# Kernel tuning notes

Hardware: AMD Instinct MI355X
Metric: run time of the kernel (lower is better)

Reference implementation:

```python
import jax, jax.numpy as jnp
import numpy as np

B, S = 1, 1024
V_SZ, D, L, H, DK, DV = 50304, 768, 12, 24, 32, 32
EPS = 1e-5


def layernorm(x, g, b):
    m = jnp.mean(x, axis=-1, keepdims=True)
    v = jnp.mean((x - m) ** 2, axis=-1, keepdims=True)
    return (x - m) * jax.lax.rsqrt(v + EPS) * g + b


def setup_inputs() -> dict:
    key = jax.random.key(0)
    ks = jax.random.split(key, 8)
    s = 0.02
    qkv_out = H * (DK + DK + DV)
    return {
        "token_ids": jax.random.randint(ks[0], (B, S), 0, V_SZ),
        "embed_w": (jax.random.uniform(ks[1], (V_SZ, D), minval=-1.0, maxval=1.0) / np.float32(np.sqrt(D))).astype(jnp.float32),
        "pos_w": jax.random.normal(ks[2], (D, 2 * D), dtype=jnp.float32) * s,
        "pos_b": jnp.zeros((2 * D,), jnp.float32),
        "ln1_g": jnp.ones((L, D), jnp.float32),
        "ln1_b": jnp.zeros((L, D), jnp.float32),
        "qkv_w": jax.random.normal(ks[3], (L, D, qkv_out), dtype=jnp.float32) * s,
        "qkv_b": jnp.zeros((L, qkv_out), jnp.float32),
        "ff_w1": jax.random.normal(ks[4], (L, H * DV, 2 * D), dtype=jnp.float32) * s,
        "ff_b1": jnp.zeros((L, 2 * D), jnp.float32),
        "ff_w2": jax.random.normal(ks[5], (L, D, D), dtype=jnp.float32) * s,
        "lnf_g": jnp.ones((D,), jnp.float32),
        "lnf_b": jnp.zeros((D,), jnp.float32),
    }


def _embed_position(x, pos_w, pos_b):
    # Heinsen log-linear recurrence (arXiv:2311.06281), using_prev_context=False.
    h = x @ pos_w + pos_b                     # [B,S,2D]
    log_coeffs = jax.nn.log_sigmoid(h[..., :D])
    logits = h[..., D:]
    a_star = jnp.pad(jnp.cumsum(log_coeffs, axis=1), ((0, 0), (1, 0), (0, 0)))  # [B,S+1,D]
    prepended = jnp.pad(logits, ((0, 0), (1, 0), (0, 0)))                        # logit0 = 0
    rec = a_star + jax.lax.cumlogsumexp(prepended - a_star, axis=1)
    return x + rec[:, 1:, :]


def _layer(x, p):
    g1, b1, wqkv, bqkv, w1, bb1, w2 = p
    y = layernorm(x, g1, b1) @ wqkv + bqkv                  # [B,S,H*(2DK+DV)]
    y = y.reshape(B, S, H, DK + DK + DV).transpose(0, 2, 1, 3)  # [B,H,S,.]
    Q, K, V = y[..., :DK], y[..., DK:2 * DK], y[..., 2 * DK:]
    # Heinsen log-domain causal attention (arXiv:2404.05843)
    H_S = jax.lax.cumlogsumexp(K[..., :, None] + V[..., None, :], axis=2)  # [B,H,S,DK,DV]
    H_Z = jax.lax.cumlogsumexp(K, axis=2)                                   # [B,H,S,DK]
    log_S = jax.nn.logsumexp(Q[..., None] + H_S, axis=-2)                   # [B,H,S,DV]
    log_Z = jax.nn.logsumexp(Q + H_Z, axis=-1, keepdims=True)               # [B,H,S,1]
    att = (log_S - log_Z).transpose(0, 2, 1, 3).reshape(B, S, H * DV)
    z = att @ w1 + bb1                                       # [B,S,2D]
    z = z[..., :D] * jax.nn.sigmoid(z[..., D:])              # GLU(dim=-1)
    z = z @ w2
    return x + z, None


def reference(token_ids, embed_w, pos_w, pos_b, ln1_g, ln1_b, qkv_w, qkv_b, ff_w1, ff_b1, ff_w2, lnf_g, lnf_b):
    x = embed_w[token_ids]                                   # [B,S,D]
    x = _embed_position(x, pos_w, pos_b)
    x, _ = jax.lax.scan(_layer, x, (ln1_g, ln1_b, qkv_w, qkv_b, ff_w1, ff_b1, ff_w2))
    x = layernorm(x, lnf_g, lnf_b)
    return x @ embed_w.T                                     # [B,S,V_SZ]
```

## Files before the change

kernel.cpp:

```cpp
#include <hip/hip_runtime.h>
#include <math.h>

#define S 1024
#define D 768
#define L 12
#define NH 24
#define QKV_OUT 2304
#define FF1_OUT 1536
#define V_SZ 50304

typedef unsigned short u16;
typedef __attribute__((ext_vector_type(8))) short bf16x8;
typedef __attribute__((ext_vector_type(4))) float f32x4;

__device__ __forceinline__ u16 f2bf(float x) {
    unsigned u = __float_as_uint(x);
    u += 0x7fffu + ((u >> 16) & 1u);
    return (u16)(u >> 16);
}

__device__ __forceinline__ void async_copy16(const void* g, void* l) {
    __builtin_amdgcn_global_load_lds(
        (const __attribute__((address_space(1))) unsigned int*)g,
        (__attribute__((address_space(3))) unsigned int*)l, 16, 0, 0);
}

__global__ __launch_bounds__(256) void embed_kernel(
    const int* __restrict__ tok, const float* __restrict__ ew,
    float* __restrict__ x, u16* __restrict__ xb) {
    int t = blockIdx.x;
    int id = tok[t];
    const float* src = ew + (size_t)id * D;
    for (int d = threadIdx.x; d < D; d += 256) {
        float v = src[d];
        x[(size_t)t * D + d] = v;
        xb[(size_t)t * D + d] = f2bf(v);
    }
}

__global__ __launch_bounds__(256) void cvt_bf16_kernel(
    const float* __restrict__ in, u16* __restrict__ out) {
    size_t i = ((size_t)blockIdx.x * 256 + threadIdx.x) * 8;
    float4 a = *(const float4*)(in + i);
    float4 b = *(const float4*)(in + i + 4);
    uint4 o;
    o.x = (unsigned)f2bf(a.x) | ((unsigned)f2bf(a.y) << 16);
    o.y = (unsigned)f2bf(a.z) | ((unsigned)f2bf(a.w) << 16);
    o.z = (unsigned)f2bf(b.x) | ((unsigned)f2bf(b.y) << 16);
    o.w = (unsigned)f2bf(b.z) | ((unsigned)f2bf(b.w) << 16);
    *(uint4*)(out + i) = o;
}

__global__ __launch_bounds__(256) void pos_scan_kernel(
    const float* __restrict__ h, float* __restrict__ x) {
    const int d = blockIdx.x;
    const int tid = threadIdx.x;
    float a[4], b[4];
    #pragma unroll
    for (int i = 0; i < 4; ++i) {
        int t = tid * 4 + i;
        float g  = h[(size_t)t * FF1_OUT + d];
        float lg = h[(size_t)t * FF1_OUT + D + d];
        a[i] = 1.f / (1.f + __expf(-g));
        b[i] = __expf(lg);
    }
    float A = ((a[0] * a[1]) * a[2]) * a[3];
    float B = ((b[0] * a[1] + b[1]) * a[2] + b[2]) * a[3] + b[3];

    __shared__ float sA[256], sB[256];
    sA[tid] = A; sB[tid] = B;
    __syncthreads();
    #pragma unroll
    for (int off = 1; off < 256; off <<= 1) {
        float selfA = sA[tid], selfB = sB[tid];
        float pA = 1.f, pB = 0.f;
        if (tid >= off) { pA = sA[tid - off]; pB = sB[tid - off]; }
        __syncthreads();
        sA[tid] = pA * selfA;
        sB[tid] = pB * selfA + selfB;
        __syncthreads();
    }
    float R = 1.f;
    if (tid > 0) R = sA[tid - 1] + sB[tid - 1];
    #pragma unroll
    for (int i = 0; i < 4; ++i) {
        R = R * a[i] + b[i];
        x[(size_t)(tid * 4 + i) * D + d] += __logf(R);
    }
}

__global__ __launch_bounds__(256) void ln_kernel(
    const float* __restrict__ in, const float* __restrict__ g,
    const float* __restrict__ b, u16* __restrict__ out) {
    int row = blockIdx.x;
    int tid = threadIdx.x;
    const float* p = in + (size_t)row * D;
    float v0 = p[tid], v1 = p[tid + 256], v2 = p[tid + 512];

    __shared__ float red[8];
    float s = v0 + v1 + v2;
    #pragma unroll
    for (int o = 32; o > 0; o >>= 1) s += __shfl_down(s, o, 64);
    int wave = tid >> 6, lane = tid & 63;
    if (lane == 0) red[wave] = s;
    __syncthreads();
    float mean = (red[0] + red[1] + red[2] + red[3]) * (1.f / (float)D);

    float d0 = v0 - mean, d1 = v1 - mean, d2 = v2 - mean;
    float ss = d0 * d0 + d1 * d1 + d2 * d2;
    #pragma unroll
    for (int o = 32; o > 0; o >>= 1) ss += __shfl_down(ss, o, 64);
    if (lane == 0) red[4 + wave] = ss;
    __syncthreads();
    float var = (red[4] + red[5] + red[6] + red[7]) * (1.f / (float)D);
    float rstd = rsqrtf(var + 1e-5f);

    u16* o = out + (size_t)row * D;
    o[tid]       = f2bf(d0 * rstd * g[tid]       + b[tid]);
    o[tid + 256] = f2bf(d1 * rstd * g[tid + 256] + b[tid + 256]);
    o[tid + 512] = f2bf(d2 * rstd * g[tid + 512] + b[tid + 512]);
}

__global__ __launch_bounds__(256) void wconv_kernel(
    const float* __restrict__ W, u16* __restrict__ WT, int N) {
    __shared__ float tile[32][33];
    const int z = blockIdx.z;
    W  += (size_t)z * 768 * N;
    WT += (size_t)z * N * 768;
    const int n0 = blockIdx.x * 32, k0 = blockIdx.y * 32;
    const int t = threadIdx.x;
    const int r = t >> 3, c4 = (t & 7) * 4;
    float4 v = *(const float4*)(W + (size_t)(k0 + r) * N + n0 + c4);
    tile[r][c4] = v.x; tile[r][c4 + 1] = v.y; tile[r][c4 + 2] = v.z; tile[r][c4 + 3] = v.w;
    __syncthreads();
    ushort4 o;
    o.x = f2bf(tile[c4][r]);     o.y = f2bf(tile[c4 + 1][r]);
    o.z = f2bf(tile[c4 + 2][r]); o.w = f2bf(tile[c4 + 3][r]);
    *(ushort4*)(WT + (size_t)(n0 + r) * 768 + k0 + c4) = o;
}

template <bool XSWZ>
__global__ __launch_bounds__(256) void gemm_bf16_kernel(
    const u16* __restrict__ A, const u16* __restrict__ B,
    const float* __restrict__ bias, const float* __restrict__ Cin,
    float* __restrict__ C, int N) {
    constexpr int K = 768;
    __shared__ __align__(16) u16 As[128 * 32];
    __shared__ __align__(16) u16 Bs[128 * 32];
    const int tid = threadIdx.x;
    const int w = tid >> 6, lane = tid & 63;
    int m0, n0;
    if (XSWZ) {
        const int lid = blockIdx.x;
        const int xcd = lid & 7, local = lid >> 3;
        const int work = xcd * 393 + local;
        n0 = (work >> 3) * 128;
        m0 = (work & 7) * 128;
    } else {
        m0 = blockIdx.y * 128;
        n0 = blockIdx.x * 128;
    }
    const int wm = (w >> 1) * 64, wn = (w & 1) * 64;

    f32x4 acc[4][4] = {};

    const int rA = w * 32 + (lane >> 2);
    const int cA = (lane & 3) * 8;
    const int frow = lane & 15;
    const int fko = (lane >> 4) * 8;

    for (int k0 = 0; k0 < K; k0 += 32) {
        {
            const u16* g0 = A + (size_t)(m0 + rA) * K + k0 + cA;
            async_copy16(g0, (char*)As + w * 2048);
            async_copy16(g0 + (size_t)16 * K, (char*)As + w * 2048 + 1024);
        }
        {
            const u16* g0 = B + (size_t)(n0 + rA) * K + k0 + cA;
            async_copy16(g0, (char*)Bs + w * 2048);
            async_copy16(g0 + (size_t)16 * K, (char*)Bs + w * 2048 + 1024);
        }
        __syncthreads();

        bf16x8 af[4], bfr[4];
        #pragma unroll
        for (int i = 0; i < 4; ++i)
            af[i] = *(const bf16x8*)(As + (wm + i * 16 + frow) * 32 + fko);
        #pragma unroll
        for (int j = 0; j < 4; ++j)
            bfr[j] = *(const bf16x8*)(Bs + (wn + j * 16 + frow) * 32 + fko);
        #pragma unroll
        for (int i = 0; i < 4; ++i)
            #pragma unroll
            for (int j = 0; j < 4; ++j)
                acc[i][j] = __builtin_amdgcn_mfma_f32_16x16x32_bf16(af[i], bfr[j], acc[i][j], 0, 0, 0);
        __syncthreads();
    }

    const int crow = wm + (lane >> 4) * 4;
    const int ccol = wn + (lane & 15);
    #pragma unroll
    for (int j = 0; j < 4; ++j) {
        int col = n0 + ccol + j * 16;
        float bj = bias ? bias[col] : 0.f;
        #pragma unroll
        for (int i = 0; i < 4; ++i) {
            #pragma unroll
            for (int r = 0; r < 4; ++r) {
                int row = m0 + crow + i * 16 + r;
                size_t off = (size_t)row * N + col;
                float v = acc[i][j][r] + bj;
                if (Cin) v += Cin[off];
                C[off] = v;
            }
        }
    }
}

__global__ __launch_bounds__(256) void gemm_f32b_kernel(
    const u16* __restrict__ A, const float* __restrict__ B,
    const float* __restrict__ bias, const float* __restrict__ Cin,
    float* __restrict__ C, int N) {
    constexpr int K = 768;
    __shared__ __align__(16) u16 As[128 * 32];
    __shared__ __align__(16) u16 Bs[128 * 32];
    const int tid = threadIdx.x;
    const int w = tid >> 6, lane = tid & 63;
    const int m0 = blockIdx.y * 128, n0 = blockIdx.x * 128;
    const int wm = (w >> 1) * 64, wn = (w & 1) * 64;

    f32x4 acc[4][4] = {};

    const int rA = w * 32 + (lane >> 2);
    const int cA = (lane & 3) * 8;
    const int frow = lane & 15;
    const int fko = (lane >> 4) * 8;

    for (int k0 = 0; k0 < K; k0 += 32) {
        {
            const u16* g0 = A + (size_t)(m0 + rA) * K + k0 + cA;
            async_copy16(g0, (char*)As + w * 2048);
            async_copy16(g0 + (size_t)16 * K, (char*)As + w * 2048 + 1024);
        }
        {
            const int r = tid >> 1, half = tid & 1;
            const float* src = B + (size_t)(n0 + r) * K + k0 + half * 16;
            float4 v0 = *(const float4*)(src);
            float4 v1 = *(const float4*)(src + 4);
            float4 v2 = *(const float4*)(src + 8);
            float4 v3 = *(const float4*)(src + 12);
            unsigned p0 = (unsigned)f2bf(v0.x) | ((unsigned)f2bf(v0.y) << 16);
            unsigned p1 = (unsigned)f2bf(v0.z) | ((unsigned)f2bf(v0.w) << 16);
            unsigned p2 = (unsigned)f2bf(v1.x) | ((unsigned)f2bf(v1.y) << 16);
            unsigned p3 = (unsigned)f2bf(v1.z) | ((unsigned)f2bf(v1.w) << 16);
            unsigned p4 = (unsigned)f2bf(v2.x) | ((unsigned)f2bf(v2.y) << 16);
            unsigned p5 = (unsigned)f2bf(v2.z) | ((unsigned)f2bf(v2.w) << 16);
            unsigned p6 = (unsigned)f2bf(v3.x) | ((unsigned)f2bf(v3.y) << 16);
            unsigned p7 = (unsigned)f2bf(v3.z) | ((unsigned)f2bf(v3.w) << 16);
            u16* dst = Bs + r * 32 + half * 16;
            *(uint4*)(dst)     = make_uint4(p0, p1, p2, p3);
            *(uint4*)(dst + 8) = make_uint4(p4, p5, p6, p7);
        }
        __syncthreads();

        bf16x8 af[4], bfr[4];
        #pragma unroll
        for (int i = 0; i < 4; ++i)
            af[i] = *(const bf16x8*)(As + (wm + i * 16 + frow) * 32 + fko);
        #pragma unroll
        for (int j = 0; j < 4; ++j)
            bfr[j] = *(const bf16x8*)(Bs + (wn + j * 16 + frow) * 32 + fko);
        #pragma unroll
        for (int i = 0; i < 4; ++i)
            #pragma unroll
            for (int j = 0; j < 4; ++j)
                acc[i][j] = __builtin_amdgcn_mfma_f32_16x16x32_bf16(af[i], bfr[j], acc[i][j], 0, 0, 0);
        __syncthreads();
    }

    const int crow = wm + (lane >> 4) * 4;
    const int ccol = wn + (lane & 15);
    #pragma unroll
    for (int j = 0; j < 4; ++j) {
        int col = n0 + ccol + j * 16;
        float bj = bias ? bias[col] : 0.f;
        #pragma unroll
        for (int i = 0; i < 4; ++i) {
            #pragma unroll
            for (int r = 0; r < 4; ++r) {
                int row = m0 + crow + i * 16 + r;
                size_t off = (size_t)row * N + col;
                float v = acc[i][j][r] + bj;
                if (Cin) v += Cin[off];
                C[off] = v;
            }
        }
    }
}

__global__ __launch_bounds__(256) void ekv_kernel(
    const float* __restrict__ y, u16* __restrict__ ekv) {
    const int t = blockIdx.x;
    #pragma unroll
    for (int i = 0; i < 2; ++i) {
        int e = threadIdx.x + i * 256;
        int off = e * 4;
        if (off < NH * 64) {
            int h = off >> 6, c = off & 63;
            float4 v = *(const float4*)(y + (size_t)t * QKV_OUT + h * 96 + 32 + c);
            ushort4 o;
            o.x = f2bf(__expf(v.x)); o.y = f2bf(__expf(v.y));
            o.z = f2bf(__expf(v.z)); o.w = f2bf(__expf(v.w));
            *(ushort4*)(ekv + (size_t)t * (NH * 64) + off) = o;
        }
    }
}

__global__ __launch_bounds__(256) void attn_kernel(
    const float* __restrict__ y, const u16* __restrict__ ekv,
    u16* __restrict__ att) {
    const int tb = blockIdx.x, head = blockIdx.y;
    const int tid = threadIdx.x, w = tid >> 6, lane = tid & 63;
    const int q = lane >> 4, cl = lane & 15;
    const int t0 = tb * 64;

    __shared__ __align__(16) u16 Qs[64 * 32];
    __shared__ __align__(16) u16 Ks[64 * 32];
    __shared__ __align__(16) u16 Vt[32 * 64];
    __shared__ __align__(16) u16 As[4][16 * 64];
    u16* As_w = As[w];

    bf16x8 ones8;
    #pragma unroll
    for (int i = 0; i < 8; ++i) ones8[i] = (short)0x3F80;

    f32x4 accO[2] = {};
    f32x4 accZ = {};

    #pragma unroll
    for (int i = 0; i < 2; ++i) {
        int e = tid + i * 256;
        int row = e >> 3, c4 = (e & 7) * 4;
        float4 v = *(const float4*)(y + (size_t)(t0 + row) * QKV_OUT + head * 96 + c4);
        ushort4 o;
        o.x = f2bf(__expf(v.x)); o.y = f2bf(__expf(v.y));
        o.z = f2bf(__expf(v.z)); o.w = f2bf(__expf(v.w));
        *(ushort4*)(Qs + row * 32 + c4) = o;
    }

    for (int sb = 0; sb <= tb; ++sb) {
        const int s0 = sb * 64;
        #pragma unroll
        for (int i = 0; i < 2; ++i) {
            int e = tid + i * 256;
            int row = e >> 3, c4 = (e & 7) * 4;
            const u16* src = ekv + (size_t)(s0 + row) * (NH * 64) + head * 64;
            ushort4 k4 = *(const ushort4*)(src + c4);
            *(ushort4*)(Ks + row * 32 + c4) = k4;
            ushort4 v4 = *(const ushort4*)(src + 32 + c4);
            u16 vv[4] = {v4.x, v4.y, v4.z, v4.w};
            #pragma unroll
            for (int n = 0; n < 4; ++n) {
                int j = c4 + n;
                Vt[j * 64 + (((row >> 4) ^ (j & 3)) * 16) + (row & 15)] = vv[n];
            }
        }
        __syncthreads();

        bf16x8 af_q = *(const bf16x8*)(Qs + (w * 16 + cl) * 32 + q * 8);
        f32x4 aqk[4];
        #pragma unroll
        for (int nt = 0; nt < 4; ++nt) {
            bf16x8 bk = *(const bf16x8*)(Ks + (nt * 16 + cl) * 32 + q * 8);
            aqk[nt] = __builtin_amdgcn_mfma_f32_16x16x32_bf16(af_q, bk, (f32x4){0.f, 0.f, 0.f, 0.f}, 0, 0, 0);
        }
        #pragma unroll
        for (int nt = 0; nt < 4; ++nt) {
            #pragma unroll
            for (int reg = 0; reg < 4; ++reg) {
                int r = q * 4 + reg;
                int tg = t0 + w * 16 + r;
                int cg = s0 + nt * 16 + cl;
                float v = (cg <= tg) ? aqk[nt][reg] : 0.f;
                As_w[r * 64 + ((nt ^ q) * 16) + cl] = f2bf(v);
            }
        }
        bf16x8 af_a[2];
        #pragma unroll
        for (int kt = 0; kt < 2; ++kt) {
            int blk = (kt * 2 + (q >> 1)) ^ (cl >> 2);
            af_a[kt] = *(const bf16x8*)(As_w + cl * 64 + blk * 16 + (q & 1) * 8);
        }
        #pragma unroll
        for (int kt = 0; kt < 2; ++kt)
            accZ = __builtin_amdgcn_mfma_f32_16x16x32_bf16(af_a[kt], ones8, accZ, 0, 0, 0);
        #pragma unroll
        for (int nt = 0; nt < 2; ++nt) {
            #pragma unroll
            for (int kt = 0; kt < 2; ++kt) {
                int j = nt * 16 + cl;
                int blk = (kt * 2 + (q >> 1)) ^ (j & 3);
                bf16x8 bv = *(const bf16x8*)(Vt + j * 64 + blk * 16 + (q & 1) * 8);
                accO[nt] = __builtin_amdgcn_mfma_f32_16x16x32_bf16(af_a[kt], bv, accO[nt], 0, 0, 0);
            }
        }
        __syncthreads();
    }

    #pragma unroll
    for (int nt = 0; nt < 2; ++nt) {
        #pragma unroll
        for (int reg = 0; reg < 4; ++reg) {
            int t = t0 + w * 16 + q * 4 + reg;
            int j = nt * 16 + cl;
            att[(size_t)t * D + head * 32 + j] = f2bf(__logf(accO[nt][reg]) - __logf(accZ[reg]));
        }
    }
}

__global__ __launch_bounds__(256) void glu_kernel(
    const float* __restrict__ z, u16* __restrict__ zg) {
    int idx = blockIdx.x * 256 + threadIdx.x;
    int t = idx / D, d = idx - t * D;
    float a = z[(size_t)t * FF1_OUT + d];
    float g = z[(size_t)t * FF1_OUT + D + d];
    zg[idx] = f2bf(a * (1.f / (1.f + __expf(-g))));
}

extern "C" void kernel_launch(void* const* d_in, const int* in_sizes, int n_in,
                              void* d_out, int out_size, void* d_ws, size_t ws_size,
                              hipStream_t stream) {
    const int*   tok     = (const int*)d_in[0];
    const float* embed_w = (const float*)d_in[1];
    const float* pos_w   = (const float*)d_in[2];
    const float* pos_b   = (const float*)d_in[3];
    const float* ln1_g   = (const float*)d_in[4];
    const float* ln1_b   = (const float*)d_in[5];
    const float* qkv_w   = (const float*)d_in[6];
    const float* qkv_b   = (const float*)d_in[7];
    const float* ff_w1   = (const float*)d_in[8];
    const float* ff_b1   = (const float*)d_in[9];
    const float* ff_w2   = (const float*)d_in[10];
    const float* lnf_g   = (const float*)d_in[11];
    const float* lnf_b   = (const float*)d_in[12];
    float* out = (float*)d_out;

    char* base = (char*)d_ws;
    float* X    = (float*)(base);
    u16*   XB   = (u16*)  (base + 3145728);
    float* Y    = (float*)(base + 4718592);
    u16*   LNX  = (u16*)  (base + 14155776);
    u16*   ATT  = (u16*)  (base + 15728640);
    u16*   ZG   = (u16*)  (base + 17301504);
    u16*   posT = (u16*)  (base + 18874368);
    u16*   qkvT = (u16*)  (base + 21233664);
    u16*   ff1T = (u16*)  (base + 63700992);
    u16*   ff2T = (u16*)  (base + 92012544);
    u16*   EBW  = (u16*)  (base + 106168320);
    u16*   EKV  = (u16*)  (base + 106168320);
    const bool bf16_head = ws_size >= (size_t)106168320 + 77266944;

    wconv_kernel<<<dim3(48, 24, 1),  256, 0, stream>>>(pos_w, posT, 1536);
    wconv_kernel<<<dim3(72, 24, 12), 256, 0, stream>>>(qkv_w, qkvT, 2304);
    wconv_kernel<<<dim3(48, 24, 12), 256, 0, stream>>>(ff_w1, ff1T, 1536);
    wconv_kernel<<<dim3(24, 24, 12), 256, 0, stream>>>(ff_w2, ff2T, 768);

    embed_kernel<<<S, 256, 0, stream>>>(tok, embed_w, X, XB);

    gemm_bf16_kernel<false><<<dim3(12, 8), 256, 0, stream>>>(XB, posT, pos_b, nullptr, Y, FF1_OUT);
    pos_scan_kernel<<<D, 256, 0, stream>>>(Y, X);

    for (int l = 0; l < L; ++l) {
        ln_kernel<<<S, 256, 0, stream>>>(X, ln1_g + (size_t)l * D, ln1_b + (size_t)l * D, LNX);
        gemm_bf16_kernel<false><<<dim3(18, 8), 256, 0, stream>>>(
            LNX, qkvT + (size_t)l * QKV_OUT * 768, qkv_b + (size_t)l * QKV_OUT, nullptr, Y, QKV_OUT);
        ekv_kernel<<<S, 256, 0, stream>>>(Y, EKV);
        attn_kernel<<<dim3(16, NH), 256, 0, stream>>>(Y, EKV, ATT);
        gemm_bf16_kernel<false><<<dim3(12, 8), 256, 0, stream>>>(
            ATT, ff1T + (size_t)l * FF1_OUT * 768, ff_b1 + (size_t)l * FF1_OUT, nullptr, Y, FF1_OUT);
        glu_kernel<<<(S * D) / 256, 256, 0, stream>>>(Y, ZG);
        gemm_bf16_kernel<false><<<dim3(6, 8), 256, 0, stream>>>(
            ZG, ff2T + (size_t)l * D * 768, nullptr, X, X, D);
    }

    ln_kernel<<<S, 256, 0, stream>>>(X, lnf_g, lnf_b, LNX);
    if (bf16_head) {
        cvt_bf16_kernel<<<18864, 256, 0, stream>>>(embed_w, EBW);
        gemm_bf16_kernel<true><<<dim3(3144), 256, 0, stream>>>(LNX, EBW, nullptr, nullptr, out, V_SZ);
    } else {
        gemm_f32b_kernel<<<dim3(393, 8), 256, 0, stream>>>(LNX, embed_w, nullptr, nullptr, out, V_SZ);
    }
}
```

Measured before the change: 1.913 ms.

## Fuse exp into QKV GEMM epilogue, GLU into FF2 prologue, use 64x64 tiles

The GEMM kernel is now templated on tile size, with two optional fusions. The QKV projection writes exp(y) as bf16 directly, which removes the separate ekv kernel and the fp32 Y round trip for Q/K/V. The FF2 GEMM computes the GLU from the fp32 FF1 output while loading its A tile, which removes the glu kernel and the ZG buffer. The per-layer GEMMs switch to 64x64 tiles so more blocks cover the CUs, and the LM head drops its XCD swizzle for a plain 2D grid. The costs are redundant GLU computation across N tiles, synchronous loads in the fused prologue, and possible L2 locality loss on the head GEMM.

```diff
diff --git a/kernel.cpp b/kernel.cpp
--- a/kernel.cpp
+++ b/kernel.cpp
@@ -139,79 +139,101 @@
     *(ushort4*)(WT + (size_t)(n0 + r) * 768 + k0 + c4) = o;
 }
 
-template <bool XSWZ>
+template <int BM, int BN, bool GLUA, bool EXPOUT>
 __global__ __launch_bounds__(256) void gemm_bf16_kernel(
-    const u16* __restrict__ A, const u16* __restrict__ B,
-    const float* __restrict__ bias, const float* __restrict__ Cin,
-    float* __restrict__ C, int N) {
+    const u16* __restrict__ A, const float* __restrict__ Af,
+    const u16* __restrict__ B, const float* __restrict__ bias,
+    const float* __restrict__ Cin, float* __restrict__ C,
+    u16* __restrict__ E, int N) {
     constexpr int K = 768;
-    __shared__ __align__(16) u16 As[128 * 32];
-    __shared__ __align__(16) u16 Bs[128 * 32];
+    constexpr int MI = BM / 32;
+    constexpr int NI = BN / 32;
+    __shared__ __align__(16) u16 As[BM * 32];
+    __shared__ __align__(16) u16 Bs[BN * 32];
     const int tid = threadIdx.x;
     const int w = tid >> 6, lane = tid & 63;
-    int m0, n0;
-    if (XSWZ) {
-        const int lid = blockIdx.x;
-        const int xcd = lid & 7, local = lid >> 3;
-        const int work = xcd * 393 + local;
-        n0 = (work >> 3) * 128;
-        m0 = (work & 7) * 128;
-    } else {
-        m0 = blockIdx.y * 128;
-        n0 = blockIdx.x * 128;
-    }
-    const int wm = (w >> 1) * 64, wn = (w & 1) * 64;
-
-    f32x4 acc[4][4] = {};
-
-    const int rA = w * 32 + (lane >> 2);
-    const int cA = (lane & 3) * 8;
+    const int m0 = blockIdx.y * BM, n0 = blockIdx.x * BN;
+    const int wm = (w >> 1) * (BM / 2);
+    const int wn = (w & 1) * (BN / 2);
+
+    f32x4 acc[MI][NI] = {};
     const int frow = lane & 15;
     const int fko = (lane >> 4) * 8;
 
     for (int k0 = 0; k0 < K; k0 += 32) {
+        if constexpr (GLUA) {
+            const int r = tid >> 2, c8 = (tid & 3) * 8;
+            const float* pa = Af + (size_t)(m0 + r) * FF1_OUT + k0 + c8;
+            float4 a0 = *(const float4*)(pa);
+            float4 a1 = *(const float4*)(pa + 4);
+            float4 g0 = *(const float4*)(pa + D);
+            float4 g1 = *(const float4*)(pa + D + 4);
+            float o0 = a0.x / (1.f + __expf(-g0.x));
+            float o1 = a0.y / (1.f + __expf(-g0.y));
+            float o2 = a0.z / (1.f + __expf(-g0.z));
+            float o3 = a0.w / (1.f + __expf(-g0.w));
+            float o4 = a1.x / (1.f + __expf(-g1.x));
+            float o5 = a1.y / (1.f + __expf(-g1.y));
+            float o6 = a1.z / (1.f + __expf(-g1.z));
+            float o7 = a1.w / (1.f + __expf(-g1.w));
+            uint4 st;
+            st.x = (unsigned)f2bf(o0) | ((unsigned)f2bf(o1) << 16);
+            st.y = (unsigned)f2bf(o2) | ((unsigned)f2bf(o3) << 16);
+            st.z = (unsigned)f2bf(o4) | ((unsigned)f2bf(o5) << 16);
+            st.w = (unsigned)f2bf(o6) | ((unsigned)f2bf(o7) << 16);
+            *(uint4*)(As + r * 32 + c8) = st;
+        } else {
+            const int rA = w * (BM / 4) + (lane >> 2);
+            const int cA = (lane & 3) * 8;
+            const u16* g0 = A + (size_t)(m0 + rA) * K + k0 + cA;
+            async_copy16(g0, (char*)As + w * (BM * 16));
+            if constexpr (BM == 128)
+                async_copy16(g0 + (size_t)16 * K, (char*)As + w * (BM * 16) + 1024);
+        }
         {
-            const u16* g0 = A + (size_t)(m0 + rA) * K + k0 + cA;
-            async_copy16(g0, (char*)As + w * 2048);
-            async_copy16(g0 + (size_t)16 * K, (char*)As + w * 2048 + 1024);
-        }
-        {
-            const u16* g0 = B + (size_t)(n0 + rA) * K + k0 + cA;
-            async_copy16(g0, (char*)Bs + w * 2048);
-            async_copy16(g0 + (size_t)16 * K, (char*)Bs + w * 2048 + 1024);
-        }
-        __syncthreads();
-
-        bf16x8 af[4], bfr[4];
-        #pragma unroll
-        for (int i = 0; i < 4; ++i)
+            const int rB = w * (BN / 4) + (lane >> 2);
+            const int cB = (lane & 3) * 8;
+            const u16* g0 = B + (size_t)(n0 + rB) * K + k0 + cB;
+            async_copy16(g0, (char*)Bs + w * (BN * 16));
+            if constexpr (BN == 128)
+                async_copy16(g0 + (size_t)16 * K, (char*)Bs + w * (BN * 16) + 1024);
+        }
+        __syncthreads();
+
+        bf16x8 af[MI], bfr[NI];
+        #pragma unroll
+        for (int i = 0; i < MI; ++i)
             af[i] = *(const bf16x8*)(As + (wm + i * 16 + frow) * 32 + fko);
         #pragma unroll
-        for (int j = 0; j < 4; ++j)
+        for (int j = 0; j < NI; ++j)
             bfr[j] = *(const bf16x8*)(Bs + (wn + j * 16 + frow) * 32 + fko);
         #pragma unroll
-        for (int i = 0; i < 4; ++i)
-            #pragma unroll
-            for (int j = 0; j < 4; ++j)
+        for (int i = 0; i < MI; ++i)
+            #pragma unroll
+            for (int j = 0; j < NI; ++j)
                 acc[i][j] = __builtin_amdgcn_mfma_f32_16x16x32_bf16(af[i], bfr[j], acc[i][j], 0, 0, 0);
         __syncthreads();
     }
 
-    const int crow = wm + (lane >> 4) * 4;
-    const int ccol = wn + (lane & 15);
-    #pragma unroll
-    for (int j = 0; j < 4; ++j) {
-        int col = n0 + ccol + j * 16;
+    const int crow4 = (lane >> 4) * 4;
+    const int ccol = lane & 15;
+    #pragma unroll
+    for (int j = 0; j < NI; ++j) {
+        int col = n0 + wn + j * 16 + ccol;
         float bj = bias ? bias[col] : 0.f;
         #pragma unroll
-        for (int i = 0; i < 4; ++i) {
+        for (int i = 0; i < MI; ++i) {
             #pragma unroll
             for (int r = 0; r < 4; ++r) {
-                int row = m0 + crow + i * 16 + r;
+                int row = m0 + wm + i * 16 + crow4 + r;
                 size_t off = (size_t)row * N + col;
                 float v = acc[i][j][r] + bj;
-                if (Cin) v += Cin[off];
-                C[off] = v;
+                if constexpr (EXPOUT) {
+                    E[off] = f2bf(__expf(v));
+                } else {
+                    if (Cin) v += Cin[off];
+                    C[off] = v;
+                }
             }
         }
     }
@@ -298,27 +320,8 @@
     }
 }
 
-__global__ __launch_bounds__(256) void ekv_kernel(
-    const float* __restrict__ y, u16* __restrict__ ekv) {
-    const int t = blockIdx.x;
-    #pragma unroll
-    for (int i = 0; i < 2; ++i) {
-        int e = threadIdx.x + i * 256;
-        int off = e * 4;
-        if (off < NH * 64) {
-            int h = off >> 6, c = off & 63;
-            float4 v = *(const float4*)(y + (size_t)t * QKV_OUT + h * 96 + 32 + c);
-            ushort4 o;
-            o.x = f2bf(__expf(v.x)); o.y = f2bf(__expf(v.y));
-            o.z = f2bf(__expf(v.z)); o.w = f2bf(__expf(v.w));
-            *(ushort4*)(ekv + (size_t)t * (NH * 64) + off) = o;
-        }
-    }
-}
-
 __global__ __launch_bounds__(256) void attn_kernel(
-    const float* __restrict__ y, const u16* __restrict__ ekv,
-    u16* __restrict__ att) {
+    const u16* __restrict__ eq, u16* __restrict__ att) {
     const int tb = blockIdx.x, head = blockIdx.y;
     const int tid = threadIdx.x, w = tid >> 6, lane = tid & 63;
     const int q = lane >> 4, cl = lane & 15;
@@ -337,27 +340,24 @@
     f32x4 accO[2] = {};
     f32x4 accZ = {};
 
-    #pragma unroll
-    for (int i = 0; i < 2; ++i) {
-        int e = tid + i * 256;
-        int row = e >> 3, c4 = (e & 7) * 4;
-        float4 v = *(const float4*)(y + (size_t)(t0 + row) * QKV_OUT + head * 96 + c4);
-        ushort4 o;
-        o.x = f2bf(__expf(v.x)); o.y = f2bf(__expf(v.y));
-        o.z = f2bf(__expf(v.z)); o.w = f2bf(__expf(v.w));
-        *(ushort4*)(Qs + row * 32 + c4) = o;
+    {
+        int row = tid >> 2, c8 = (tid & 3) * 8;
+        *(bf16x8*)(Qs + row * 32 + c8) =
+            *(const bf16x8*)(eq + (size_t)(t0 + row) * QKV_OUT + head * 96 + c8);
     }
 
     for (int sb = 0; sb <= tb; ++sb) {
         const int s0 = sb * 64;
+        {
+            int row = tid >> 2, c8 = (tid & 3) * 8;
+            *(bf16x8*)(Ks + row * 32 + c8) =
+                *(const bf16x8*)(eq + (size_t)(s0 + row) * QKV_OUT + head * 96 + 32 + c8);
+        }
         #pragma unroll
         for (int i = 0; i < 2; ++i) {
             int e = tid + i * 256;
             int row = e >> 3, c4 = (e & 7) * 4;
-            const u16* src = ekv + (size_t)(s0 + row) * (NH * 64) + head * 64;
-            ushort4 k4 = *(const ushort4*)(src + c4);
-            *(ushort4*)(Ks + row * 32 + c4) = k4;
-            ushort4 v4 = *(const ushort4*)(src + 32 + c4);
+            ushort4 v4 = *(const ushort4*)(eq + (size_t)(s0 + row) * QKV_OUT + head * 96 + 64 + c4);
             u16 vv[4] = {v4.x, v4.y, v4.z, v4.w};
             #pragma unroll
             for (int n = 0; n < 4; ++n) {
@@ -416,15 +416,6 @@
             att[(size_t)t * D + head * 32 + j] = f2bf(__logf(accO[nt][reg]) - __logf(accZ[reg]));
         }
     }
-}
-
-__global__ __launch_bounds__(256) void glu_kernel(
-    const float* __restrict__ z, u16* __restrict__ zg) {
-    int idx = blockIdx.x * 256 + threadIdx.x;
-    int t = idx / D, d = idx - t * D;
-    float a = z[(size_t)t * FF1_OUT + d];
-    float g = z[(size_t)t * FF1_OUT + D + d];
-    zg[idx] = f2bf(a * (1.f / (1.f + __expf(-g))));
 }
 
 extern "C" void kernel_launch(void* const* d_in, const int* in_sizes, int n_in,
@@ -451,13 +442,12 @@
     float* Y    = (float*)(base + 4718592);
     u16*   LNX  = (u16*)  (base + 14155776);
     u16*   ATT  = (u16*)  (base + 15728640);
-    u16*   ZG   = (u16*)  (base + 17301504);
     u16*   posT = (u16*)  (base + 18874368);
     u16*   qkvT = (u16*)  (base + 21233664);
     u16*   ff1T = (u16*)  (base + 63700992);
     u16*   ff2T = (u16*)  (base + 92012544);
+    u16*   EQKV = (u16*)  (base + 106168320);
     u16*   EBW  = (u16*)  (base + 106168320);
-    u16*   EKV  = (u16*)  (base + 106168320);
     const bool bf16_head = ws_size >= (size_t)106168320 + 77266944;
 
     wconv_kernel<<<dim3(48, 24, 1),  256, 0, stream>>>(pos_w, posT, 1536);
@@ -467,26 +457,28 @@
 
     embed_kernel<<<S, 256, 0, stream>>>(tok, embed_w, X, XB);
 
-    gemm_bf16_kernel<false><<<dim3(12, 8), 256, 0, stream>>>(XB, posT, pos_b, nullptr, Y, FF1_OUT);
+    gemm_bf16_kernel<64, 64, false, false><<<dim3(24, 16), 256, 0, stream>>>(
+        XB, nullptr, posT, pos_b, nullptr, Y, nullptr, FF1_OUT);
     pos_scan_kernel<<<D, 256, 0, stream>>>(Y, X);
 
     for (int l = 0; l < L; ++l) {
         ln_kernel<<<S, 256, 0, stream>>>(X, ln1_g + (size_t)l * D, ln1_b + (size_t)l * D, LNX);
-        gemm_bf16_kernel<false><<<dim3(18, 8), 256, 0, stream>>>(
-            LNX, qkvT + (size_t)l * QKV_OUT * 768, qkv_b + (size_t)l * QKV_OUT, nullptr, Y, QKV_OUT);
-        ekv_kernel<<<S, 256, 0, stream>>>(Y, EKV);
-        attn_kernel<<<dim3(16, NH), 256, 0, stream>>>(Y, EKV, ATT);
-        gemm_bf16_kernel<false><<<dim3(12, 8), 256, 0, stream>>>(
-            ATT, ff1T + (size_t)l * FF1_OUT * 768, ff_b1 + (size_t)l * FF1_OUT, nullptr, Y, FF1_OUT);
-        glu_kernel<<<(S * D) / 256, 256, 0, stream>>>(Y, ZG);
-        gemm_bf16_kernel<false><<<dim3(6, 8), 256, 0, stream>>>(
-            ZG, ff2T + (size_t)l * D * 768, nullptr, X, X, D);
+        gemm_bf16_kernel<64, 64, false, true><<<dim3(36, 16), 256, 0, stream>>>(
+            LNX, nullptr, qkvT + (size_t)l * QKV_OUT * 768, qkv_b + (size_t)l * QKV_OUT,
+            nullptr, nullptr, EQKV, QKV_OUT);
+        attn_kernel<<<dim3(16, NH), 256, 0, stream>>>(EQKV, ATT);
+        gemm_bf16_kernel<64, 64, false, false><<<dim3(24, 16), 256, 0, stream>>>(
+            ATT, nullptr, ff1T + (size_t)l * FF1_OUT * 768, ff_b1 + (size_t)l * FF1_OUT,
+            nullptr, Y, nullptr, FF1_OUT);
+        gemm_bf16_kernel<64, 64, true, false><<<dim3(12, 16), 256, 0, stream>>>(
+            nullptr, Y, ff2T + (size_t)l * D * 768, nullptr, X, X, nullptr, D);
     }
 
     ln_kernel<<<S, 256, 0, stream>>>(X, lnf_g, lnf_b, LNX);
     if (bf16_head) {
         cvt_bf16_kernel<<<18864, 256, 0, stream>>>(embed_w, EBW);
-        gemm_bf16_kernel<true><<<dim3(3144), 256, 0, stream>>>(LNX, EBW, nullptr, nullptr, out, V_SZ);
+        gemm_bf16_kernel<128, 128, false, false><<<dim3(393, 8), 256, 0, stream>>>(
+            LNX, nullptr, EBW, nullptr, nullptr, out, nullptr, V_SZ);
     } else {
         gemm_f32b_kernel<<<dim3(393, 8), 256, 0, stream>>>(LNX, embed_w, nullptr, nullptr, out, V_SZ);
     }
```

New measurement: 1.623 ms. -15.2%, faster.
